# Kernel tuning notes

Hardware: AMD Instinct MI355X
Metric: run time of the kernel (lower is better)

## Reference

```python
import jax, jax.numpy as jnp
import numpy as np

N = 48000      # total nodes
R = 16         # topological rounds
NPR = 3000     # nodes per round
DEG = 2        # children (incoming edges) per parent node
EPR = NPR * DEG
H = 128        # h_size
X = 128        # x_size
G = 16         # graphs in batch
PG = N // G    # nodes per graph == max_node_num


def setup_inputs() -> dict:
    key = jax.random.key(0)
    ks = jax.random.split(key, 8)
    j = np.arange(NPR)
    # round r parents are nodes [r*NPR,(r+1)*NPR); children come from round r-1
    edges = []
    for r in range(1, R):
        src = r * NPR + np.repeat(j, DEG)                                  # parent (edge_index[0])
        dst = (r - 1) * NPR + np.stack([j, (j + 1) % NPR], 1).ravel()       # child  (edge_index[1])
        edges.append(np.stack([src, dst], 0))
    edges_r = jnp.asarray(np.stack(edges, 0), dtype=jnp.int32)             # [R-1, 2, EPR]
    order_r = jnp.asarray(np.stack([r * NPR + j for r in range(1, R)], 0), dtype=jnp.int32)  # [R-1, NPR]
    order0 = jnp.asarray(j, dtype=jnp.int32)                               # leaves, round 0
    graph_idx = jnp.asarray(np.arange(N) // PG, dtype=jnp.int32)
    pos_idx = jnp.asarray(np.arange(N) % PG, dtype=jnp.int32)
    s = jnp.float32(0.05)
    return {
        'x': jax.random.normal(ks[0], (N, X), jnp.float32),
        'edge_labels_r': jax.random.randint(ks[1], (R - 1, EPR, 1), 0, 2).astype(jnp.float32),
        'W_iou': jax.random.normal(ks[2], (3 * H, X), jnp.float32) * s,
        'W_f': jax.random.normal(ks[3], (H, X), jnp.float32) * s,
        'b_iou': jax.random.normal(ks[4], (1, 3 * H), jnp.float32) * s,
        'b_f': jax.random.normal(ks[5], (1, H), jnp.float32) * s,
        'U_iou': jax.random.normal(ks[6], (3 * H, 2 * H), jnp.float32) * s,
        'U_f': jax.random.normal(ks[7], (H, 2 * H), jnp.float32) * s,
        'edges_r': edges_r,
        'order0': order0,
        'order_r': order_r,
        'graph_idx': graph_idx,
        'pos_idx': pos_idx,
        'graph_num': G,
        'max_node_num': PG,
    }


def reference(x, edge_labels_r, W_iou, W_f, b_iou, b_f, U_iou, U_f,
              edges_r, order0, order_r, graph_idx, pos_idx, graph_num, max_node_num):
    n = x.shape[0]
    h_size = W_f.shape[0]
    iou_x = x @ W_iou.T    # [n, 3h]
    wf_x = x @ W_f.T       # [n, h]

    def node_update(h, c, iou_mid, order):
        iou = iou_x[order] + iou_mid[order] + b_iou
        i, o, u = jnp.split(iou, 3, axis=1)
        c_temp = jax.nn.sigmoid(i) * jnp.tanh(u) + c[order]
        c = c.at[order].set(c_temp)
        h = h.at[order].set(jax.nn.sigmoid(o) * jnp.tanh(c_temp))
        return h, c

    h = jnp.zeros((n, h_size), x.dtype)
    c = jnp.zeros_like(h)
    iou_mid = jnp.zeros((n, 3 * h_size), x.dtype)
    h, c = node_update(h, c, iou_mid, order0)

    def step(carry, inp):
        h, c, iou_mid = carry
        edges, lab, order = inp        # edges [2,EPR], lab [EPR,1], order [NPR]
        src, child = edges[0], edges[1]
        h_j = h[child]
        # h_t0 (label==0 part) first, then h_t1, matching torch cat order
        h_two = jnp.concatenate([(1.0 - lab) * h_j, lab * h_j], axis=1)   # [EPR, 2h]
        iou_mid = iou_mid.at[src].add(h_two @ U_iou.T)
        f = jax.nn.sigmoid(wf_x[child] + h_two @ U_f.T + b_f)
        c = c.at[src].add(f * jnp.clip(c[child], -1e14, 1e14))
        h, c = node_update(h, c, iou_mid, order)
        return (h, c, iou_mid), None

    (h, c, iou_mid), _ = jax.lax.scan(step, (h, c, iou_mid), (edges_r, edge_labels_r, order_r))

    h_out = jnp.zeros((graph_num, max_node_num, h_size), x.dtype)
    return h_out.at[graph_idx, pos_idx].set(h)
```

## Files before the change

### kernel.cpp

```cpp
#include <hip/hip_runtime.h>
#include <math.h>

#define NN   48000
#define RR   16
#define NPR  3000
#define EPR  6000
#define HH   128
#define XX   128
#define C512 512

#define PPB  12
#define NB   250
#define MAXP 27
#define MAXE 52

typedef __attribute__((ext_vector_type(8))) short short8;
typedef __attribute__((ext_vector_type(8))) unsigned short ushort8;
typedef __attribute__((ext_vector_type(4))) float f32x4;

__device__ __forceinline__ float sigm(float v) {
  return __fdividef(1.0f, 1.0f + __expf(-v));
}
__device__ __forceinline__ float tanh_fast(float v) {
  return 1.0f - 2.0f * __fdividef(1.0f, 1.0f + __expf(2.0f * v));
}
__device__ __forceinline__ float clampc(float v) {
  return fminf(fmaxf(v, -1e14f), 1e14f);
}
__device__ __forceinline__ unsigned short f2bf(float f) {
  unsigned int u = __float_as_uint(f);
  unsigned int r = (u + 0x7FFFu + ((u >> 16) & 1u)) >> 16;
  return (unsigned short)r;
}

__global__ __launch_bounds__(256) void prep_wu(
    const float* __restrict__ Wiou, const float* __restrict__ Wf,
    const float* __restrict__ Uiou, const float* __restrict__ Uf,
    const float* __restrict__ b_iou, const float* __restrict__ b_f,
    unsigned short* __restrict__ Wbf, unsigned short* __restrict__ Ubf,
    float* __restrict__ biof) {
  int t = blockIdx.x * 256 + threadIdx.x;
  if (t < 512) biof[t] = (t < 384) ? b_iou[t] : b_f[t - 384];
  if (t < 512 * 128) {
    int r = t >> 7, c = t & 127;
    float v = (r < 384) ? Wiou[r * 128 + c] : Wf[(r - 384) * 128 + c];
    Wbf[t] = f2bf(v);
  }
  if (t < 512 * 256) {
    int r = t >> 8, c = t & 255;
    float v = (r < 384) ? Uiou[r * 256 + c] : Uf[(r - 384) * 256 + c];
    Ubf[t] = f2bf(v);
  }
}

__global__ __launch_bounds__(256) void pre_gemm_mfma(
    const float* __restrict__ x, const unsigned short* __restrict__ Wbf,
    const float* __restrict__ biof, float* __restrict__ pre) {
  __shared__ __align__(16) unsigned short A[128][136];
  __shared__ __align__(16) float T[128][132];
  const int n0 = blockIdx.x * 128;
  const int t = threadIdx.x;

#pragma unroll
  for (int pass = 0; pass < 4; ++pass) {
    int row = (t >> 3) + pass * 32;
    int cb = (t & 7) * 16;
    const float* src = x + (size_t)(n0 + row) * XX + cb;
    unsigned short hv[16];
#pragma unroll
    for (int i = 0; i < 16; i += 4) {
      float4 v = *(const float4*)(src + i);
      hv[i] = f2bf(v.x); hv[i + 1] = f2bf(v.y);
      hv[i + 2] = f2bf(v.z); hv[i + 3] = f2bf(v.w);
    }
    *(ushort8*)&A[row][cb] = *(ushort8*)&hv[0];
    *(ushort8*)&A[row][cb + 8] = *(ushort8*)&hv[8];
  }
  __syncthreads();

  const int wave = t >> 6, lane = t & 63;
  const int wk = (wave & 1) * 64;
  const int wn = (wave >> 1) * 64;
  const int ln = lane & 15, q = lane >> 4;

  for (int ko = 0; ko < 4; ++ko) {
    const int k0 = ko * 128;
    f32x4 acc[4][4];
#pragma unroll
    for (int mt = 0; mt < 4; ++mt)
#pragma unroll
      for (int nt = 0; nt < 4; ++nt)
        acc[mt][nt] = (f32x4){0.f, 0.f, 0.f, 0.f};

#pragma unroll
    for (int kt = 0; kt < 4; ++kt) {
      short8 af[4], bfr[4];
#pragma unroll
      for (int mt = 0; mt < 4; ++mt)
        af[mt] = *(const short8*)(Wbf +
            (size_t)(k0 + wk + mt * 16 + ln) * 128 + kt * 32 + q * 8);
#pragma unroll
      for (int nt = 0; nt < 4; ++nt)
        bfr[nt] = *(const short8*)&A[wn + nt * 16 + ln][kt * 32 + q * 8];
#pragma unroll
      for (int mt = 0; mt < 4; ++mt)
#pragma unroll
        for (int nt = 0; nt < 4; ++nt)
          acc[mt][nt] = __builtin_amdgcn_mfma_f32_16x16x32_bf16(
              af[mt], bfr[nt], acc[mt][nt], 0, 0, 0);
    }

    if (ko) __syncthreads();
#pragma unroll
    for (int mt = 0; mt < 4; ++mt)
#pragma unroll
      for (int nt = 0; nt < 4; ++nt) {
        float4 o;
        o.x = acc[mt][nt][0]; o.y = acc[mt][nt][1];
        o.z = acc[mt][nt][2]; o.w = acc[mt][nt][3];
        *(float4*)&T[wn + nt * 16 + ln][wk + mt * 16 + q * 4] = o;
      }
    __syncthreads();

    {
      int row0 = t >> 5;
      int seg = t & 31;
      float4 bv = *(const float4*)(biof + k0 + seg * 4);
#pragma unroll
      for (int rp = 0; rp < 16; ++rp) {
        int row = rp * 8 + row0;
        float4 v = *(const float4*)&T[row][seg * 4];
        float4 o;
        o.x = v.x + bv.x; o.y = v.y + bv.y;
        o.z = v.z + bv.z; o.w = v.w + bv.w;
        *(float4*)(pre + (size_t)(n0 + row) * C512 + k0 + seg * 4) = o;
      }
    }
  }
}

__global__ __launch_bounds__(1024, 4) void rounds_halo(
    const float* __restrict__ pre, const unsigned short* __restrict__ Ubf,
    const float* __restrict__ labels, const int* __restrict__ order0,
    const int* __restrict__ order_r, float* __restrict__ hout) {
  __shared__ float Cp[2][MAXP + 1][132];
  __shared__ unsigned char labA[15 * 56];
  __shared__ int ordA[16 * 28];
  __shared__ __align__(16) unsigned short Abuf[56][264];
  __shared__ float Sb[26][392];
  __shared__ float Fb[52][132];

  const int t = threadIdx.x;
  const int b = blockIdx.x;
  const int g0 = b * PPB;
  const int w = t >> 6, lane = t & 63;
  const int ln = lane & 15, q = lane >> 4;

  if (t < 15 * 56) {
    int rr = t / 56, e = t - rr * 56;
    int p = e >> 1;
    int gp = g0 + p; if (gp >= NPR) gp -= NPR;
    labA[t] = (labels[(size_t)rr * EPR + 2 * gp + (e & 1)] >= 0.5f) ? 1 : 0;
  }
  if (t < 16 * 28) {
    int rr = t / 28, p = t - rr * 28;
    int gp = g0 + p; if (gp >= NPR) gp -= NPR;
    ordA[t] = (rr == 0) ? order0[gp] : order_r[(size_t)(rr - 1) * NPR + gp];
  }
  __syncthreads();

  const unsigned short* const ubase = Ubf + (size_t)(w * 32 + ln) * 256 + q * 8;

#pragma unroll
  for (int i = 0; i < 4; ++i) {
    int idx = t + i * 1024;
    int row = idx >> 7, j = idx & 127;
    if (row < MAXP) {
      int n = ordA[row];
      const float* pr = pre + (size_t)n * C512;
      float ct = sigm(pr[j]) * tanh_fast(pr[256 + j]);
      float ht = sigm(pr[128 + j]) * tanh_fast(ct);
      Cp[0][row][j] = ct;
      unsigned short hb = f2bf(ht);
      int L0 = labA[2 * row];
      Abuf[2 * row][j + (L0 ? 128 : 0)] = hb;
      Abuf[2 * row][j + (L0 ? 0 : 128)] = 0;
      if (row >= 1) {
        int L1 = labA[2 * row - 1];
        Abuf[2 * row - 1][j + (L1 ? 128 : 0)] = hb;
        Abuf[2 * row - 1][j + (L1 ? 0 : 128)] = 0;
      }
      if (row < PPB) hout[(size_t)n * HH + j] = ht;
    }
  }

  for (int r = 1; r < RR; ++r) {
    const int prv = (r - 1) & 1, cur = r & 1;
    const int Pr = MAXP - r;
    const int Er = 2 * Pr;
    const int NT = (Er + 15) >> 4;
    const int NIv = (Pr + 7) >> 3;

    __syncthreads();

    f32x4 acc[4][2];
#pragma unroll
    for (int mt = 0; mt < 4; ++mt)
#pragma unroll
      for (int nt = 0; nt < 2; ++nt)
        acc[mt][nt] = (f32x4){0.f, 0.f, 0.f, 0.f};

    short8 cb0 = *(const short8*)(ubase);
    short8 cb1 = *(const short8*)(ubase + (size_t)(16 * 256));
#pragma unroll
    for (int kt = 0; kt < 8; ++kt) {
      short8 nb0 = cb0, nb1 = cb1;
      if (kt < 7) {
        nb0 = *(const short8*)(ubase + (size_t)(kt + 1) * 32);
        nb1 = *(const short8*)(ubase + (size_t)(16 * 256) + (kt + 1) * 32);
      }
#pragma unroll
      for (int mt = 0; mt < 4; ++mt) {
        if (mt < NT) {
          short8 af = *(const short8*)&Abuf[mt * 16 + ln][kt * 32 + q * 8];
          acc[mt][0] = __builtin_amdgcn_mfma_f32_16x16x32_bf16(
              af, cb0, acc[mt][0], 0, 0, 0);
          acc[mt][1] = __builtin_amdgcn_mfma_f32_16x16x32_bf16(
              af, cb1, acc[mt][1], 0, 0, 0);
        }
      }
      cb0 = nb0; cb1 = nb1;
    }

#pragma unroll
    for (int mt = 0; mt < 4; ++mt) {
      if (mt < NT) {
#pragma unroll
        for (int nt = 0; nt < 2; ++nt) {
          int colg = w * 32 + nt * 16 + ln;
          if (colg < 384) {
#pragma unroll
            for (int rs = 0; rs < 2; ++rs) {
              int prow = mt * 8 + q * 2 + rs;
              if (prow < Pr)
                Sb[prow][colg] = acc[mt][nt][2 * rs] + acc[mt][nt][2 * rs + 1];
            }
          } else {
#pragma unroll
            for (int rr2 = 0; rr2 < 4; ++rr2) {
              int erow = mt * 16 + q * 4 + rr2;
              if (erow < Er) Fb[erow][colg - 384] = acc[mt][nt][rr2];
            }
          }
        }
      }
    }
    __syncthreads();

#pragma unroll
    for (int i = 0; i < 4; ++i) {
      if (i < NIv) {
        int idx = t + i * 1024;
        int p = idx >> 7, j = idx & 127;
        if (p < Pr) {
          int n  = ordA[r * 28 + p];
          int n0 = ordA[(r - 1) * 28 + p];
          int n1 = ordA[(r - 1) * 28 + p + 1];
          const float* pr = pre + (size_t)n * C512;
          float gi = pr[j] + Sb[p][j];
          float go = pr[128 + j] + Sb[p][128 + j];
          float gu = pr[256 + j] + Sb[p][256 + j];
          float wf0 = pre[(size_t)n0 * C512 + 384 + j];
          float wf1 = pre[(size_t)n1 * C512 + 384 + j];
          float f0 = sigm(wf0 + Fb[2 * p][j]);
          float f1 = sigm(wf1 + Fb[2 * p + 1][j]);
          float facc = f0 * clampc(Cp[prv][p][j]) +
                       f1 * clampc(Cp[prv][p + 1][j]);
          float ct = sigm(gi) * tanh_fast(gu) + facc;
          float ht = sigm(go) * tanh_fast(ct);
          Cp[cur][p][j] = ct;
          unsigned short hb = f2bf(ht);
          if (r < RR - 1) {
            int L0 = labA[r * 56 + 2 * p];
            Abuf[2 * p][j + (L0 ? 128 : 0)] = hb;
            Abuf[2 * p][j + (L0 ? 0 : 128)] = 0;
            if (p >= 1) {
              int L1 = labA[r * 56 + 2 * p - 1];
              Abuf[2 * p - 1][j + (L1 ? 128 : 0)] = hb;
              Abuf[2 * p - 1][j + (L1 ? 0 : 128)] = 0;
            }
          }
          if (p < PPB) hout[(size_t)n * HH + j] = ht;
        }
      }
    }
  }
}

extern "C" void kernel_launch(void* const* d_in, const int* in_sizes, int n_in,
                              void* d_out, int out_size, void* d_ws, size_t ws_size,
                              hipStream_t stream) {
  const float* x       = (const float*)d_in[0];
  const float* labels  = (const float*)d_in[1];
  const float* Wiou    = (const float*)d_in[2];
  const float* Wf      = (const float*)d_in[3];
  const float* b_iou   = (const float*)d_in[4];
  const float* b_f     = (const float*)d_in[5];
  const float* Uiou    = (const float*)d_in[6];
  const float* Uf      = (const float*)d_in[7];
  const int*   order0  = (const int*)d_in[9];
  const int*   order_r = (const int*)d_in[10];

  float* hout = (float*)d_out;

  float* pre  = (float*)d_ws;
  unsigned short* Wbf = (unsigned short*)(pre + (size_t)NN * C512);
  unsigned short* Ubf = Wbf + 512 * 128;
  float* biof = (float*)(Ubf + 512 * 256);

  prep_wu<<<512, 256, 0, stream>>>(Wiou, Wf, Uiou, Uf, b_iou, b_f,
                                   Wbf, Ubf, biof);
  pre_gemm_mfma<<<NN / 128, 256, 0, stream>>>(x, Wbf, biof, pre);
  rounds_halo<<<NB, 1024, 0, stream>>>(pre, Ubf, labels, order0, order_r,
                                       hout);
}
```

Baseline: 326.8 us.

## Halve per-block halo tile, use 512 threads, store partial sums as bf16

Each block in the recurrent rounds kernel now owns 6 parents instead of 12, so the grid grows to 500 blocks of 512 threads and the halo shrinks to 21 nodes. Each wave now computes 64 output columns with four B fragments per k-step, which replaces the double-buffered two-column prefetch. The gate and forget partial sums in shared memory are now stored as bf16, which cuts LDS use and may let more blocks fit per CU. The costs are more redundant halo recomputation relative to useful work and some added rounding error in the pre-activation sums.

New measurement: 713.2 us. 2.18x slower.

```diff
diff --git a/kernel.cpp b/kernel.cpp
--- a/kernel.cpp
+++ b/kernel.cpp
@@ -9,10 +9,10 @@
 #define XX   128
 #define C512 512
 
-#define PPB  12
-#define NB   250
-#define MAXP 27
-#define MAXE 52
+#define PPB  6
+#define NB   500
+#define MAXP 21
+#define MAXE 40
 
 typedef __attribute__((ext_vector_type(8))) short short8;
 typedef __attribute__((ext_vector_type(8))) unsigned short ushort8;
@@ -31,6 +31,9 @@
   unsigned int u = __float_as_uint(f);
   unsigned int r = (u + 0x7FFFu + ((u >> 16) & 1u)) >> 16;
   return (unsigned short)r;
+}
+__device__ __forceinline__ float bf2f(unsigned short h) {
+  return __uint_as_float(((unsigned int)h) << 16);
 }
 
 __global__ __launch_bounds__(256) void prep_wu(
@@ -139,16 +142,16 @@
   }
 }
 
-__global__ __launch_bounds__(1024, 4) void rounds_halo(
+__global__ __launch_bounds__(512, 4) void rounds_halo(
     const float* __restrict__ pre, const unsigned short* __restrict__ Ubf,
     const float* __restrict__ labels, const int* __restrict__ order0,
     const int* __restrict__ order_r, float* __restrict__ hout) {
   __shared__ float Cp[2][MAXP + 1][132];
-  __shared__ unsigned char labA[15 * 56];
-  __shared__ int ordA[16 * 28];
-  __shared__ __align__(16) unsigned short Abuf[56][264];
-  __shared__ float Sb[26][392];
-  __shared__ float Fb[52][132];
+  __shared__ unsigned char labA[15 * MAXE];
+  __shared__ int ordA[16 * 22];
+  __shared__ __align__(16) unsigned short Abuf[48][264];
+  __shared__ unsigned short Sb[20][394];
+  __shared__ unsigned short Fb[40][132];
 
   const int t = threadIdx.x;
   const int b = blockIdx.x;
@@ -156,24 +159,29 @@
   const int w = t >> 6, lane = t & 63;
   const int ln = lane & 15, q = lane >> 4;
 
-  if (t < 15 * 56) {
-    int rr = t / 56, e = t - rr * 56;
+  for (int i = t; i < 15 * MAXE; i += 512) {
+    int rr = i / MAXE, e = i - rr * MAXE;
     int p = e >> 1;
     int gp = g0 + p; if (gp >= NPR) gp -= NPR;
-    labA[t] = (labels[(size_t)rr * EPR + 2 * gp + (e & 1)] >= 0.5f) ? 1 : 0;
-  }
-  if (t < 16 * 28) {
-    int rr = t / 28, p = t - rr * 28;
+    labA[i] = (labels[(size_t)rr * EPR + 2 * gp + (e & 1)] >= 0.5f) ? 1 : 0;
+  }
+  if (t < 16 * 22) {
+    int rr = t / 22, p = t - rr * 22;
     int gp = g0 + p; if (gp >= NPR) gp -= NPR;
     ordA[t] = (rr == 0) ? order0[gp] : order_r[(size_t)(rr - 1) * NPR + gp];
   }
+  for (int i = t; i < 8 * 264; i += 512)
+    Abuf[40 + i / 264][i % 264] = 0;
   __syncthreads();
 
-  const unsigned short* const ubase = Ubf + (size_t)(w * 32 + ln) * 256 + q * 8;
-
-#pragma unroll
-  for (int i = 0; i < 4; ++i) {
-    int idx = t + i * 1024;
+  const unsigned short* ub[4];
+#pragma unroll
+  for (int nt = 0; nt < 4; ++nt)
+    ub[nt] = Ubf + (size_t)(w * 64 + nt * 16 + ln) * 256 + q * 8;
+
+#pragma unroll
+  for (int i = 0; i < 6; ++i) {
+    int idx = t + i * 512;
     int row = idx >> 7, j = idx & 127;
     if (row < MAXP) {
       int n = ordA[row];
@@ -199,57 +207,54 @@
     const int Pr = MAXP - r;
     const int Er = 2 * Pr;
     const int NT = (Er + 15) >> 4;
-    const int NIv = (Pr + 7) >> 3;
+    const int NIv = (Pr + 3) >> 2;
 
     __syncthreads();
 
-    f32x4 acc[4][2];
-#pragma unroll
-    for (int mt = 0; mt < 4; ++mt)
-#pragma unroll
-      for (int nt = 0; nt < 2; ++nt)
+    f32x4 acc[3][4];
+#pragma unroll
+    for (int mt = 0; mt < 3; ++mt)
+#pragma unroll
+      for (int nt = 0; nt < 4; ++nt)
         acc[mt][nt] = (f32x4){0.f, 0.f, 0.f, 0.f};
 
-    short8 cb0 = *(const short8*)(ubase);
-    short8 cb1 = *(const short8*)(ubase + (size_t)(16 * 256));
 #pragma unroll
     for (int kt = 0; kt < 8; ++kt) {
-      short8 nb0 = cb0, nb1 = cb1;
-      if (kt < 7) {
-        nb0 = *(const short8*)(ubase + (size_t)(kt + 1) * 32);
-        nb1 = *(const short8*)(ubase + (size_t)(16 * 256) + (kt + 1) * 32);
-      }
-#pragma unroll
-      for (int mt = 0; mt < 4; ++mt) {
+      short8 bv[4];
+#pragma unroll
+      for (int nt = 0; nt < 4; ++nt)
+        bv[nt] = *(const short8*)(ub[nt] + (size_t)kt * 32);
+#pragma unroll
+      for (int mt = 0; mt < 3; ++mt) {
         if (mt < NT) {
           short8 af = *(const short8*)&Abuf[mt * 16 + ln][kt * 32 + q * 8];
-          acc[mt][0] = __builtin_amdgcn_mfma_f32_16x16x32_bf16(
-              af, cb0, acc[mt][0], 0, 0, 0);
-          acc[mt][1] = __builtin_amdgcn_mfma_f32_16x16x32_bf16(
-              af, cb1, acc[mt][1], 0, 0, 0);
+#pragma unroll
+          for (int nt = 0; nt < 4; ++nt)
+            acc[mt][nt] = __builtin_amdgcn_mfma_f32_16x16x32_bf16(
+                af, bv[nt], acc[mt][nt], 0, 0, 0);
         }
       }
-      cb0 = nb0; cb1 = nb1;
-    }
-
-#pragma unroll
-    for (int mt = 0; mt < 4; ++mt) {
+    }
+
+#pragma unroll
+    for (int mt = 0; mt < 3; ++mt) {
       if (mt < NT) {
 #pragma unroll
-        for (int nt = 0; nt < 2; ++nt) {
-          int colg = w * 32 + nt * 16 + ln;
+        for (int nt = 0; nt < 4; ++nt) {
+          int colg = w * 64 + nt * 16 + ln;
           if (colg < 384) {
 #pragma unroll
             for (int rs = 0; rs < 2; ++rs) {
               int prow = mt * 8 + q * 2 + rs;
               if (prow < Pr)
-                Sb[prow][colg] = acc[mt][nt][2 * rs] + acc[mt][nt][2 * rs + 1];
+                Sb[prow][colg] =
+                    f2bf(acc[mt][nt][2 * rs] + acc[mt][nt][2 * rs + 1]);
             }
           } else {
 #pragma unroll
-            for (int rr2 = 0; rr2 < 4; ++rr2) {
-              int erow = mt * 16 + q * 4 + rr2;
-              if (erow < Er) Fb[erow][colg - 384] = acc[mt][nt][rr2];
+            for (int reg = 0; reg < 4; ++reg) {
+              int erow = mt * 16 + q * 4 + reg;
+              if (erow < Er) Fb[erow][colg - 384] = f2bf(acc[mt][nt][reg]);
             }
           }
         }
@@ -258,22 +263,22 @@
     __syncthreads();
 
 #pragma unroll
-    for (int i = 0; i < 4; ++i) {
+    for (int i = 0; i < 5; ++i) {
       if (i < NIv) {
-        int idx = t + i * 1024;
+        int idx = t + i * 512;
         int p = idx >> 7, j = idx & 127;
         if (p < Pr) {
-          int n  = ordA[r * 28 + p];
-          int n0 = ordA[(r - 1) * 28 + p];
-          int n1 = ordA[(r - 1) * 28 + p + 1];
+          int n  = ordA[r * 22 + p];
+          int n0 = ordA[(r - 1) * 22 + p];
+          int n1 = ordA[(r - 1) * 22 + p + 1];
           const float* pr = pre + (size_t)n * C512;
-          float gi = pr[j] + Sb[p][j];
-          float go = pr[128 + j] + Sb[p][128 + j];
-          float gu = pr[256 + j] + Sb[p][256 + j];
+          float gi = pr[j] + bf2f(Sb[p][j]);
+          float go = pr[128 + j] + bf2f(Sb[p][128 + j]);
+          float gu = pr[256 + j] + bf2f(Sb[p][256 + j]);
           float wf0 = pre[(size_t)n0 * C512 + 384 + j];
           float wf1 = pre[(size_t)n1 * C512 + 384 + j];
-          float f0 = sigm(wf0 + Fb[2 * p][j]);
-          float f1 = sigm(wf1 + Fb[2 * p + 1][j]);
+          float f0 = sigm(wf0 + bf2f(Fb[2 * p][j]));
+          float f1 = sigm(wf1 + bf2f(Fb[2 * p + 1][j]));
           float facc = f0 * clampc(Cp[prv][p][j]) +
                        f1 * clampc(Cp[prv][p + 1][j]);
           float ct = sigm(gi) * tanh_fast(gu) + facc;
@@ -281,11 +286,11 @@
           Cp[cur][p][j] = ct;
           unsigned short hb = f2bf(ht);
           if (r < RR - 1) {
-            int L0 = labA[r * 56 + 2 * p];
+            int L0 = labA[r * MAXE + 2 * p];
             Abuf[2 * p][j + (L0 ? 128 : 0)] = hb;
             Abuf[2 * p][j + (L0 ? 0 : 128)] = 0;
             if (p >= 1) {
-              int L1 = labA[r * 56 + 2 * p - 1];
+              int L1 = labA[r * MAXE + 2 * p - 1];
               Abuf[2 * p - 1][j + (L1 ? 128 : 0)] = hb;
               Abuf[2 * p - 1][j + (L1 ? 0 : 128)] = 0;
             }
@@ -321,6 +326,6 @@
   prep_wu<<<512, 256, 0, stream>>>(Wiou, Wf, Uiou, Uf, b_iou, b_f,
                                    Wbf, Ubf, biof);
   pre_gemm_mfma<<<NN / 128, 256, 0, stream>>>(x, Wbf, biof, pre);
-  rounds_halo<<<NB, 1024, 0, stream>>>(pre, Ubf, labels, order0, order_r,
-                                       hout);
-}
+  rounds_halo<<<NB, 512, 0, stream>>>(pre, Ubf, labels, order0, order_r,
+                                      hout);
+}
```
